# Kernel tuning notes

Hardware: AMD Instinct MI355X
Metric: run time of the kernel (lower is better)

The kernel has to match this reference:

```python
import jax, jax.numpy as jnp
import numpy as np

TEMPERATURE = 2.0


def _offdiag_idx(n):
    # flat indices of the off-diagonal entries of an [n, n] matrix, row-major,
    # reshaped to [n, n-1] (matches torch masked_select(~eye).view(n, n-1))
    idx = np.arange(n * n).reshape(n, n)
    return jnp.asarray(idx[~np.eye(n, dtype=bool)].reshape(n, n - 1))


def setup_inputs() -> dict:
    key = jax.random.key(0)
    k1, k2, k3, k4 = jax.random.split(key, 4)
    B, D = 256, 512
    return {
        "wt_emb": jax.random.normal(k1, (B, D), dtype=jnp.float32),
        "mt_emb": jax.random.normal(k2, (B, D), dtype=jnp.float32),
        "label_wt": jax.random.uniform(k3, (B,), dtype=jnp.float32),
        "label_mt": jax.random.uniform(k4, (B,), dtype=jnp.float32),
    }


def reference(wt_emb, mt_emb, label_wt, label_mt):
    t = TEMPERATURE
    features = jnp.concatenate([wt_emb, mt_emb], axis=0)            # [n, D]
    labels = jnp.concatenate([label_wt, label_mt], axis=0)[:, None]  # [n, 1]
    n = features.shape[0]

    # L1 label differences: [n, n]
    label_diffs = jnp.abs(labels[:, None, :] - labels[None, :, :]).sum(-1)

    # negative L2 feature distances (safe sqrt: diagonal is exactly 0)
    diff = features[:, None, :] - features[None, :, :]               # [n, n, D]
    sq = jnp.sum(diff * diff, axis=-1)                               # [n, n]
    dist = jnp.where(sq > 0, jnp.sqrt(jnp.where(sq > 0, sq, 1.0)), 0.0)
    logits = -dist / t
    logits = logits - jax.lax.stop_gradient(jnp.max(logits, axis=1, keepdims=True))
    exp_logits = jnp.exp(logits)

    # drop diagonal -> [n, n-1]
    off = _offdiag_idx(n)
    lo = logits.reshape(-1)[off]
    eo = exp_logits.reshape(-1)[off]
    ldo = label_diffs.reshape(-1)[off]

    # vectorized over positive index k: mask[i, k, j] = ld[i, j] >= ld[i, k]
    neg_mask = ldo[:, None, :] >= ldo[:, :, None]                    # [n, n-1, n-1]
    denom = jnp.sum(jnp.where(neg_mask, eo[:, None, :], 0.0), axis=-1)  # [n, n-1]
    pos_log_probs = lo - jnp.log(denom)                              # [n, n-1]
    return -jnp.sum(pos_log_probs) / (n * (n - 1))
```

## Files before the change

### kernel.cpp

```cpp
#include <hip/hip_runtime.h>

#define N 512
#define B 256
#define D 512
#define NT 512
#define NBLK (N / 2)

#define WS_SL    0
#define WS_NORM  512
#define WS_PART  1024
#define WS_FH    2048
#define WS_G     (2048 + (N * D) / 2)

typedef _Float16 half4_t  __attribute__((ext_vector_type(4)));
typedef _Float16 half8_t  __attribute__((ext_vector_type(8)));
typedef float    f32x4    __attribute__((ext_vector_type(4)));

__global__ __launch_bounds__(NT) void sort_rows_kernel(
    const float* __restrict__ wt, const float* __restrict__ mt,
    const float* __restrict__ lwt, const float* __restrict__ lmt,
    float* __restrict__ ws)
{
    const int t = threadIdx.x, b = blockIdx.x;
    __shared__ float slab[N];
    __shared__ int scnt[32];
    slab[t] = (t < B) ? lwt[t] : lmt[t - B];
    if (t < 32) scnt[t] = 0;
    __syncthreads();

    const int jj = t & 31, j = b * 32 + jj, c = t >> 5;
    const float lj = slab[j];
    int r = 0;
    #pragma unroll 8
    for (int x = c * 32; x < c * 32 + 32; ++x) {
        const float v = slab[x];
        r += (v < lj || (v == lj && x < j)) ? 1 : 0;
    }
    atomicAdd(&scnt[jj], r);
    __syncthreads();

    if (t < 32)
        ws[WS_SL + scnt[t]] = slab[b * 32 + t];

    const int row = b * 32 + (t >> 4), s16 = t & 15;
    const int rr = scnt[t >> 4];
    const float* F = (row < B) ? (wt + (size_t)row * D) : (mt + (size_t)(row - B) * D);
    const float4* F4 = (const float4*)F;
    half4_t* Dst = (half4_t*)((_Float16*)(ws + WS_FH) + (size_t)rr * D);
    float nacc = 0.f;
    #pragma unroll
    for (int q = 0; q < 8; ++q) {
        const int idx = s16 + 16 * q;
        const float4 v = F4[idx];
        half4_t h;
        h[0] = (_Float16)v.x; h[1] = (_Float16)v.y;
        h[2] = (_Float16)v.z; h[3] = (_Float16)v.w;
        const float f0 = (float)h[0], f1 = (float)h[1];
        const float f2 = (float)h[2], f3 = (float)h[3];
        nacc += f0 * f0 + f1 * f1 + f2 * f2 + f3 * f3;
        Dst[idx] = h;
    }
    nacc += __shfl_down(nacc, 8, 16);
    nacc += __shfl_down(nacc, 4, 16);
    nacc += __shfl_down(nacc, 2, 16);
    nacc += __shfl_down(nacc, 1, 16);
    if (s16 == 0) ws[WS_NORM + rr] = nacc;
}

__global__ __launch_bounds__(256) void gram_kernel(float* __restrict__ ws)
{
    const int lane = threadIdx.x & 63;
    const int wid  = blockIdx.x * 4 + (threadIdx.x >> 6);
    const int ti = wid >> 5, tj = wid & 31;
    const int quad = lane >> 4, m = lane & 15;

    const _Float16* Fh = (const _Float16*)(ws + WS_FH);
    const _Float16* Arow = Fh + (size_t)(ti * 16 + m) * D + quad * 8;
    const _Float16* Brow = Fh + (size_t)(tj * 16 + m) * D + quad * 8;

    f32x4 acc = {0.f, 0.f, 0.f, 0.f};
    #pragma unroll
    for (int k0 = 0; k0 < D; k0 += 32) {
        const half8_t a = *(const half8_t*)(Arow + k0);
        const half8_t b = *(const half8_t*)(Brow + k0);
        acc = __builtin_amdgcn_mfma_f32_16x16x32_f16(a, b, acc, 0, 0, 0);
    }
    float* G = ws + WS_G;
    const int col = tj * 16 + m;
    #pragma unroll
    for (int rg = 0; rg < 4; ++rg)
        G[(size_t)(ti * 16 + quad * 4 + rg) * N + col] = acc[rg];
}

__global__ __launch_bounds__(NT) void rnc_main(float* __restrict__ ws)
{
    const int b = blockIdx.x, i0 = 2 * b, i1 = 2 * b + 1;
    const int t = threadIdx.x;
    const int w = t >> 6, lane = t & 63;

    __shared__ float sl[N];
    __shared__ float snm[N];
    __shared__ __align__(16) float sp0[N];
    __shared__ __align__(16) float sf0[N];
    __shared__ __align__(16) float sp1[N];
    __shared__ __align__(16) float sf1[N];
    __shared__ float sred[NT / 64];

    sl[t]  = ws[WS_SL + t];
    snm[t] = ws[WS_NORM + t];
    __syncthreads();
    const float li0 = sl[i0], li1 = sl[i1];
    const float ni0 = snm[i0], ni1 = snm[i1];

    const float* G = ws + WS_G;
    const float g0 = G[(size_t)i0 * N + t];
    const float g1 = G[(size_t)i1 * N + t];
    const float d0 = fmaxf(ni0 + snm[t] - 2.f * g0, 0.f);
    const float d1 = fmaxf(ni1 + snm[t] - 2.f * g1, 0.f);
    const float lg0 = -0.5f * sqrtf(d0);
    const float lg1 = -0.5f * sqrtf(d1);
    float lg_acc = 0.f;
    if (t != i0) lg_acc += lg0;
    if (t != i1) lg_acc += lg1;
    const float e0 = (t == i0) ? 0.f : __expf(lg0);
    const float e1 = (t == i1) ? 0.f : __expf(lg1);
    sp0[t] = e0; sf0[t] = e0;
    sp1[t] = e1; sf1[t] = e1;
    __syncthreads();

    if (w < 4) {
        float* arr = (w == 0) ? sp0 : (w == 1) ? sf0 : (w == 2) ? sp1 : sf1;
        float4* a4 = (float4*)arr;
        float4 u0 = a4[lane * 2], u1 = a4[lane * 2 + 1];
        float v0 = u0.x, v1 = u0.y, v2 = u0.z, v3 = u0.w;
        float v4 = u1.x, v5 = u1.y, v6 = u1.z, v7 = u1.w;
        if ((w & 1) == 0) {
            v1 += v0; v2 += v1; v3 += v2; v4 += v3; v5 += v4; v6 += v5; v7 += v6;
            float x = v7;
            #pragma unroll
            for (int off = 1; off < 64; off <<= 1) {
                const float y = __shfl_up(x, off, 64);
                if (lane >= off) x += y;
            }
            float ex = __shfl_up(x, 1, 64);
            if (lane == 0) ex = 0.f;
            v0 += ex; v1 += ex; v2 += ex; v3 += ex; v4 += ex; v5 += ex; v6 += ex; v7 += ex;
        } else {
            v6 += v7; v5 += v6; v4 += v5; v3 += v4; v2 += v3; v1 += v2; v0 += v1;
            float x = v0;
            #pragma unroll
            for (int off = 1; off < 64; off <<= 1) {
                const float y = __shfl_down(x, off, 64);
                if (lane + off < 64) x += y;
            }
            float ex = __shfl_down(x, 1, 64);
            if (lane == 63) ex = 0.f;
            v0 += ex; v1 += ex; v2 += ex; v3 += ex; v4 += ex; v5 += ex; v6 += ex; v7 += ex;
        }
        a4[lane * 2]     = make_float4(v0, v1, v2, v3);
        a4[lane * 2 + 1] = make_float4(v4, v5, v6, v7);
    }
    __syncthreads();

    float local = lg_acc;
    #pragma unroll
    for (int p = 0; p < 2; ++p) {
        const int x = t;
        const int ri = p ? i1 : i0;
        const float li = p ? li1 : li0;
        const float* SP = p ? sp1 : sp0;
        const float* SF = p ? sf1 : sf0;
        if (x != ri) {
            const float th = fabsf(li - sl[x]);
            int lo = 0, hi = ri + 1;
            while (lo < hi) {
                const int mid = (lo + hi) >> 1;
                if (fabsf(li - sl[mid]) >= th) lo = mid + 1; else hi = mid;
            }
            const int a = lo;
            lo = ri + 1; hi = N;
            while (lo < hi) {
                const int mid = (lo + hi) >> 1;
                if (fabsf(li - sl[mid]) >= th) hi = mid; else lo = mid + 1;
            }
            const int bb = lo;
            const float denom = ((a > 0) ? SP[a - 1] : 0.f) + ((bb < N) ? SF[bb] : 0.f);
            local -= __logf(denom);
        }
    }

    #pragma unroll
    for (int off = 32; off > 0; off >>= 1)
        local += __shfl_down(local, off, 64);
    if (lane == 0) sred[w] = local;
    __syncthreads();
    if (t == 0) {
        float sum = 0.f;
        #pragma unroll
        for (int k = 0; k < NT / 64; ++k) sum += sred[k];
        ws[WS_PART + b] = sum;
    }
}

__global__ __launch_bounds__(NBLK) void rnc_finalize(
    const float* __restrict__ ws, float* __restrict__ out)
{
    const int t = threadIdx.x;
    __shared__ float sred[NBLK / 64];
    float v = ws[WS_PART + t];
    #pragma unroll
    for (int off = 32; off > 0; off >>= 1)
        v += __shfl_down(v, off, 64);
    if ((t & 63) == 0) sred[t >> 6] = v;
    __syncthreads();
    if (t == 0) {
        float sum = 0.f;
        #pragma unroll
        for (int k = 0; k < NBLK / 64; ++k) sum += sred[k];
        out[0] = -sum / (float)((long)N * (N - 1));
    }
}

extern "C" void kernel_launch(void* const* d_in, const int* in_sizes, int n_in,
                              void* d_out, int out_size, void* d_ws, size_t ws_size,
                              hipStream_t stream) {
    const float* wt  = (const float*)d_in[0];
    const float* mt  = (const float*)d_in[1];
    const float* lwt = (const float*)d_in[2];
    const float* lmt = (const float*)d_in[3];
    float* out = (float*)d_out;
    float* ws  = (float*)d_ws;

    sort_rows_kernel<<<16, NT, 0, stream>>>(wt, mt, lwt, lmt, ws);
    gram_kernel<<<256, 256, 0, stream>>>(ws);
    rnc_main<<<NBLK, NT, 0, stream>>>(ws);
    rnc_finalize<<<1, NBLK, 0, stream>>>(ws, out);
}
```

Measured before the change: 74.84 us.

## Fuse label sort into gram kernel and finalize via atomic last-block reduction

Merges the sort/convert kernel into the gram kernel: the gram now reads fp32 features directly, converts them to fp16 in registers, and is computed in original row order. A sorted-to-original index permutation is stored so rnc_main can gather Gram entries and take norms from the Gram diagonal. The finalize kernel is replaced by an atomic accumulate plus a last-block counter inside rnc_main, cutting four launches to two. The cost is redundant fp32 loads and conversions per tile, scattered Gram gathers, and atomics.

After: 80.30 us. 7.3% more time.

```diff
diff --git a/kernel.cpp b/kernel.cpp
--- a/kernel.cpp
+++ b/kernel.cpp
@@ -3,87 +3,80 @@
 #define N 512
 #define B 256
 #define D 512
-#define NT 512
-#define NBLK (N / 2)
-
-#define WS_SL    0
-#define WS_NORM  512
-#define WS_PART  1024
-#define WS_FH    2048
-#define WS_G     (2048 + (N * D) / 2)
-
-typedef _Float16 half4_t  __attribute__((ext_vector_type(4)));
-typedef _Float16 half8_t  __attribute__((ext_vector_type(8)));
-typedef float    f32x4    __attribute__((ext_vector_type(4)));
-
-__global__ __launch_bounds__(NT) void sort_rows_kernel(
+#define NBLK 256
+
+#define WS_SL   0
+#define WS_SO   512
+#define WS_SUM  1024
+#define WS_CNT  1025
+#define WS_G    2048
+
+typedef _Float16 half8_t __attribute__((ext_vector_type(8)));
+typedef float    f32x4  __attribute__((ext_vector_type(8 / 2)));
+
+__global__ __launch_bounds__(256) void gram_rank_kernel(
     const float* __restrict__ wt, const float* __restrict__ mt,
     const float* __restrict__ lwt, const float* __restrict__ lmt,
     float* __restrict__ ws)
 {
-    const int t = threadIdx.x, b = blockIdx.x;
-    __shared__ float slab[N];
-    __shared__ int scnt[32];
-    slab[t] = (t < B) ? lwt[t] : lmt[t - B];
-    if (t < 32) scnt[t] = 0;
-    __syncthreads();
-
-    const int jj = t & 31, j = b * 32 + jj, c = t >> 5;
-    const float lj = slab[j];
-    int r = 0;
-    #pragma unroll 8
-    for (int x = c * 32; x < c * 32 + 32; ++x) {
-        const float v = slab[x];
-        r += (v < lj || (v == lj && x < j)) ? 1 : 0;
-    }
-    atomicAdd(&scnt[jj], r);
-    __syncthreads();
-
-    if (t < 32)
-        ws[WS_SL + scnt[t]] = slab[b * 32 + t];
-
-    const int row = b * 32 + (t >> 4), s16 = t & 15;
-    const int rr = scnt[t >> 4];
-    const float* F = (row < B) ? (wt + (size_t)row * D) : (mt + (size_t)(row - B) * D);
-    const float4* F4 = (const float4*)F;
-    half4_t* Dst = (half4_t*)((_Float16*)(ws + WS_FH) + (size_t)rr * D);
-    float nacc = 0.f;
-    #pragma unroll
-    for (int q = 0; q < 8; ++q) {
-        const int idx = s16 + 16 * q;
-        const float4 v = F4[idx];
-        half4_t h;
-        h[0] = (_Float16)v.x; h[1] = (_Float16)v.y;
-        h[2] = (_Float16)v.z; h[3] = (_Float16)v.w;
-        const float f0 = (float)h[0], f1 = (float)h[1];
-        const float f2 = (float)h[2], f3 = (float)h[3];
-        nacc += f0 * f0 + f1 * f1 + f2 * f2 + f3 * f3;
-        Dst[idx] = h;
-    }
-    nacc += __shfl_down(nacc, 8, 16);
-    nacc += __shfl_down(nacc, 4, 16);
-    nacc += __shfl_down(nacc, 2, 16);
-    nacc += __shfl_down(nacc, 1, 16);
-    if (s16 == 0) ws[WS_NORM + rr] = nacc;
-}
-
-__global__ __launch_bounds__(256) void gram_kernel(float* __restrict__ ws)
-{
-    const int lane = threadIdx.x & 63;
-    const int wid  = blockIdx.x * 4 + (threadIdx.x >> 6);
+    const int t = threadIdx.x, bb = blockIdx.x;
+
+    if (bb < 16) {
+        __shared__ float slab[N];
+        __shared__ int scnt[32];
+        slab[t] = (t < B) ? lwt[t] : lmt[t - B];
+        { const int t2 = t + 256; slab[t2] = (t2 < B) ? lwt[t2] : lmt[t2 - B]; }
+        if (t < 32) scnt[t] = 0;
+        __syncthreads();
+        const int jr = t >> 3, c = t & 7;
+        const int j = bb * 32 + jr;
+        const float lj = slab[j];
+        int r = 0;
+        #pragma unroll 8
+        for (int i = 0; i < 64; ++i) {
+            const int x = c + 8 * i;
+            const float v = slab[x];
+            r += (v < lj || (v == lj && x < j)) ? 1 : 0;
+        }
+        atomicAdd(&scnt[jr], r);
+        __syncthreads();
+        if (t < 32) {
+            const int r2 = scnt[t], j2 = bb * 32 + t;
+            ws[WS_SL + r2] = slab[j2];
+            ((int*)ws)[WS_SO + r2] = j2;
+        }
+        if (bb == 0 && t == 0) {
+            ws[WS_SUM] = 0.f;
+            ((unsigned*)ws)[WS_CNT] = 0u;
+        }
+    }
+
+    const int lane = t & 63;
+    const int wid  = bb * 4 + (t >> 6);
     const int ti = wid >> 5, tj = wid & 31;
     const int quad = lane >> 4, m = lane & 15;
-
-    const _Float16* Fh = (const _Float16*)(ws + WS_FH);
-    const _Float16* Arow = Fh + (size_t)(ti * 16 + m) * D + quad * 8;
-    const _Float16* Brow = Fh + (size_t)(tj * 16 + m) * D + quad * 8;
+    const int rowA = ti * 16 + m, rowB = tj * 16 + m;
+    const float* FA = (rowA < B) ? (wt + (size_t)rowA * D) : (mt + (size_t)(rowA - B) * D);
+    const float* FB = (rowB < B) ? (wt + (size_t)rowB * D) : (mt + (size_t)(rowB - B) * D);
+    FA += quad * 8; FB += quad * 8;
 
     f32x4 acc = {0.f, 0.f, 0.f, 0.f};
     #pragma unroll
     for (int k0 = 0; k0 < D; k0 += 32) {
-        const half8_t a = *(const half8_t*)(Arow + k0);
-        const half8_t b = *(const half8_t*)(Brow + k0);
-        acc = __builtin_amdgcn_mfma_f32_16x16x32_f16(a, b, acc, 0, 0, 0);
+        const float4 fa0 = *(const float4*)(FA + k0);
+        const float4 fa1 = *(const float4*)(FA + k0 + 4);
+        const float4 fb0 = *(const float4*)(FB + k0);
+        const float4 fb1 = *(const float4*)(FB + k0 + 4);
+        half8_t a, b2;
+        a[0] = (_Float16)fa0.x; a[1] = (_Float16)fa0.y;
+        a[2] = (_Float16)fa0.z; a[3] = (_Float16)fa0.w;
+        a[4] = (_Float16)fa1.x; a[5] = (_Float16)fa1.y;
+        a[6] = (_Float16)fa1.z; a[7] = (_Float16)fa1.w;
+        b2[0] = (_Float16)fb0.x; b2[1] = (_Float16)fb0.y;
+        b2[2] = (_Float16)fb0.z; b2[3] = (_Float16)fb0.w;
+        b2[4] = (_Float16)fb1.x; b2[5] = (_Float16)fb1.y;
+        b2[6] = (_Float16)fb1.z; b2[7] = (_Float16)fb1.w;
+        acc = __builtin_amdgcn_mfma_f32_16x16x32_f16(a, b2, acc, 0, 0, 0);
     }
     float* G = ws + WS_G;
     const int col = tj * 16 + m;
@@ -92,29 +85,36 @@
         G[(size_t)(ti * 16 + quad * 4 + rg) * N + col] = acc[rg];
 }
 
-__global__ __launch_bounds__(NT) void rnc_main(float* __restrict__ ws)
+__global__ __launch_bounds__(512) void rnc_main(
+    float* __restrict__ ws, float* __restrict__ out)
 {
     const int b = blockIdx.x, i0 = 2 * b, i1 = 2 * b + 1;
     const int t = threadIdx.x;
     const int w = t >> 6, lane = t & 63;
 
     __shared__ float sl[N];
+    __shared__ int   sso[N];
     __shared__ float snm[N];
     __shared__ __align__(16) float sp0[N];
     __shared__ __align__(16) float sf0[N];
     __shared__ __align__(16) float sp1[N];
     __shared__ __align__(16) float sf1[N];
-    __shared__ float sred[NT / 64];
+    __shared__ float sred[8];
 
     sl[t]  = ws[WS_SL + t];
-    snm[t] = ws[WS_NORM + t];
-    __syncthreads();
+    sso[t] = ((const int*)ws)[WS_SO + t];
+    __syncthreads();
+
+    const float* G = ws + WS_G;
+    const int ot = sso[t];
+    snm[t] = G[(size_t)ot * N + ot];
+    const int oi0 = sso[i0], oi1 = sso[i1];
     const float li0 = sl[i0], li1 = sl[i1];
+    __syncthreads();
     const float ni0 = snm[i0], ni1 = snm[i1];
 
-    const float* G = ws + WS_G;
-    const float g0 = G[(size_t)i0 * N + t];
-    const float g1 = G[(size_t)i1 * N + t];
+    const float g0 = G[(size_t)oi0 * N + ot];
+    const float g1 = G[(size_t)oi1 * N + ot];
     const float d0 = fmaxf(ni0 + snm[t] - 2.f * g0, 0.f);
     const float d1 = fmaxf(ni1 + snm[t] - 2.f * g1, 0.f);
     const float lg0 = -0.5f * sqrtf(d0);
@@ -183,8 +183,8 @@
                 const int mid = (lo + hi) >> 1;
                 if (fabsf(li - sl[mid]) >= th) hi = mid; else lo = mid + 1;
             }
-            const int bb = lo;
-            const float denom = ((a > 0) ? SP[a - 1] : 0.f) + ((bb < N) ? SF[bb] : 0.f);
+            const int bb2 = lo;
+            const float denom = ((a > 0) ? SP[a - 1] : 0.f) + ((bb2 < N) ? SF[bb2] : 0.f);
             local -= __logf(denom);
         }
     }
@@ -197,27 +197,14 @@
     if (t == 0) {
         float sum = 0.f;
         #pragma unroll
-        for (int k = 0; k < NT / 64; ++k) sum += sred[k];
-        ws[WS_PART + b] = sum;
-    }
-}
-
-__global__ __launch_bounds__(NBLK) void rnc_finalize(
-    const float* __restrict__ ws, float* __restrict__ out)
-{
-    const int t = threadIdx.x;
-    __shared__ float sred[NBLK / 64];
-    float v = ws[WS_PART + t];
-    #pragma unroll
-    for (int off = 32; off > 0; off >>= 1)
-        v += __shfl_down(v, off, 64);
-    if ((t & 63) == 0) sred[t >> 6] = v;
-    __syncthreads();
-    if (t == 0) {
-        float sum = 0.f;
-        #pragma unroll
-        for (int k = 0; k < NBLK / 64; ++k) sum += sred[k];
-        out[0] = -sum / (float)((long)N * (N - 1));
+        for (int k = 0; k < 8; ++k) sum += sred[k];
+        atomicAdd(&ws[WS_SUM], sum);
+        __threadfence();
+        const unsigned old = atomicAdd(&((unsigned*)ws)[WS_CNT], 1u);
+        if (old == NBLK - 1) {
+            const float total = atomicAdd(&ws[WS_SUM], 0.f);
+            out[0] = -total / (float)((long)N * (N - 1));
+        }
     }
 }
 
@@ -231,8 +218,6 @@
     float* out = (float*)d_out;
     float* ws  = (float*)d_ws;
 
-    sort_rows_kernel<<<16, NT, 0, stream>>>(wt, mt, lwt, lmt, ws);
-    gram_kernel<<<256, 256, 0, stream>>>(ws);
-    rnc_main<<<NBLK, NT, 0, stream>>>(ws);
-    rnc_finalize<<<1, NBLK, 0, stream>>>(ws, out);
+    gram_rank_kernel<<<256, 256, 0, stream>>>(wt, mt, lwt, lmt, ws);
+    rnc_main<<<NBLK, 512, 0, stream>>>(ws, out);
 }
```

## Fuse all stages into one cooperative kernel with grid-wide syncs

Applied to the files above, without the earlier changes.

Merges the sort, gram, main and finalize kernels into a single cooperative launch of 256 blocks, using grid.sync() between phases instead of separate kernel launches. The rank computation is redistributed so each block ranks two labels with packed warp reductions rather than the earlier per-block atomics. The goal is to remove three launch gaps. In exchange it adds the cost of cooperative launch and grid barriers, and the gram phase uses 8 waves per block with the same MFMA tiling.

New measurement: 164.5 us. +119.8%, slower.

```diff
diff --git a/kernel.cpp b/kernel.cpp
--- a/kernel.cpp
+++ b/kernel.cpp
@@ -1,10 +1,13 @@
 #include <hip/hip_runtime.h>
+#include <hip/hip_cooperative_groups.h>
+
+namespace cg = cooperative_groups;
 
 #define N 512
 #define B 256
 #define D 512
 #define NT 512
-#define NBLK (N / 2)
+#define GRID 256
 
 #define WS_SL    0
 #define WS_NORM  512
@@ -12,212 +15,219 @@
 #define WS_FH    2048
 #define WS_G     (2048 + (N * D) / 2)
 
-typedef _Float16 half4_t  __attribute__((ext_vector_type(4)));
-typedef _Float16 half8_t  __attribute__((ext_vector_type(8)));
-typedef float    f32x4    __attribute__((ext_vector_type(4)));
-
-__global__ __launch_bounds__(NT) void sort_rows_kernel(
+typedef _Float16 half8_t __attribute__((ext_vector_type(8)));
+typedef float    f32x4   __attribute__((ext_vector_type(4)));
+
+__global__ __launch_bounds__(NT) void rnc_all(
     const float* __restrict__ wt, const float* __restrict__ mt,
     const float* __restrict__ lwt, const float* __restrict__ lmt,
-    float* __restrict__ ws)
+    float* __restrict__ ws, float* __restrict__ out)
 {
-    const int t = threadIdx.x, b = blockIdx.x;
+    cg::grid_group gridg = cg::this_grid();
+    const int b = blockIdx.x, t = threadIdx.x;
+    const int w = t >> 6, lane = t & 63;
+
     __shared__ float slab[N];
-    __shared__ int scnt[32];
-    slab[t] = (t < B) ? lwt[t] : lmt[t - B];
-    if (t < 32) scnt[t] = 0;
-    __syncthreads();
-
-    const int jj = t & 31, j = b * 32 + jj, c = t >> 5;
-    const float lj = slab[j];
-    int r = 0;
-    #pragma unroll 8
-    for (int x = c * 32; x < c * 32 + 32; ++x) {
-        const float v = slab[x];
-        r += (v < lj || (v == lj && x < j)) ? 1 : 0;
-    }
-    atomicAdd(&scnt[jj], r);
-    __syncthreads();
-
-    if (t < 32)
-        ws[WS_SL + scnt[t]] = slab[b * 32 + t];
-
-    const int row = b * 32 + (t >> 4), s16 = t & 15;
-    const int rr = scnt[t >> 4];
-    const float* F = (row < B) ? (wt + (size_t)row * D) : (mt + (size_t)(row - B) * D);
-    const float4* F4 = (const float4*)F;
-    half4_t* Dst = (half4_t*)((_Float16*)(ws + WS_FH) + (size_t)rr * D);
-    float nacc = 0.f;
-    #pragma unroll
-    for (int q = 0; q < 8; ++q) {
-        const int idx = s16 + 16 * q;
-        const float4 v = F4[idx];
-        half4_t h;
-        h[0] = (_Float16)v.x; h[1] = (_Float16)v.y;
-        h[2] = (_Float16)v.z; h[3] = (_Float16)v.w;
-        const float f0 = (float)h[0], f1 = (float)h[1];
-        const float f2 = (float)h[2], f3 = (float)h[3];
-        nacc += f0 * f0 + f1 * f1 + f2 * f2 + f3 * f3;
-        Dst[idx] = h;
-    }
-    nacc += __shfl_down(nacc, 8, 16);
-    nacc += __shfl_down(nacc, 4, 16);
-    nacc += __shfl_down(nacc, 2, 16);
-    nacc += __shfl_down(nacc, 1, 16);
-    if (s16 == 0) ws[WS_NORM + rr] = nacc;
-}
-
-__global__ __launch_bounds__(256) void gram_kernel(float* __restrict__ ws)
-{
-    const int lane = threadIdx.x & 63;
-    const int wid  = blockIdx.x * 4 + (threadIdx.x >> 6);
-    const int ti = wid >> 5, tj = wid & 31;
-    const int quad = lane >> 4, m = lane & 15;
-
-    const _Float16* Fh = (const _Float16*)(ws + WS_FH);
-    const _Float16* Arow = Fh + (size_t)(ti * 16 + m) * D + quad * 8;
-    const _Float16* Brow = Fh + (size_t)(tj * 16 + m) * D + quad * 8;
-
-    f32x4 acc = {0.f, 0.f, 0.f, 0.f};
-    #pragma unroll
-    for (int k0 = 0; k0 < D; k0 += 32) {
-        const half8_t a = *(const half8_t*)(Arow + k0);
-        const half8_t b = *(const half8_t*)(Brow + k0);
-        acc = __builtin_amdgcn_mfma_f32_16x16x32_f16(a, b, acc, 0, 0, 0);
-    }
-    float* G = ws + WS_G;
-    const int col = tj * 16 + m;
-    #pragma unroll
-    for (int rg = 0; rg < 4; ++rg)
-        G[(size_t)(ti * 16 + quad * 4 + rg) * N + col] = acc[rg];
-}
-
-__global__ __launch_bounds__(NT) void rnc_main(float* __restrict__ ws)
-{
-    const int b = blockIdx.x, i0 = 2 * b, i1 = 2 * b + 1;
-    const int t = threadIdx.x;
-    const int w = t >> 6, lane = t & 63;
-
-    __shared__ float sl[N];
     __shared__ float snm[N];
     __shared__ __align__(16) float sp0[N];
     __shared__ __align__(16) float sf0[N];
     __shared__ __align__(16) float sp1[N];
     __shared__ __align__(16) float sf1[N];
-    __shared__ float sred[NT / 64];
-
-    sl[t]  = ws[WS_SL + t];
-    snm[t] = ws[WS_NORM + t];
-    __syncthreads();
-    const float li0 = sl[i0], li1 = sl[i1];
-    const float ni0 = snm[i0], ni1 = snm[i1];
-
-    const float* G = ws + WS_G;
-    const float g0 = G[(size_t)i0 * N + t];
-    const float g1 = G[(size_t)i1 * N + t];
-    const float d0 = fmaxf(ni0 + snm[t] - 2.f * g0, 0.f);
-    const float d1 = fmaxf(ni1 + snm[t] - 2.f * g1, 0.f);
-    const float lg0 = -0.5f * sqrtf(d0);
-    const float lg1 = -0.5f * sqrtf(d1);
-    float lg_acc = 0.f;
-    if (t != i0) lg_acc += lg0;
-    if (t != i1) lg_acc += lg1;
-    const float e0 = (t == i0) ? 0.f : __expf(lg0);
-    const float e1 = (t == i1) ? 0.f : __expf(lg1);
-    sp0[t] = e0; sf0[t] = e0;
-    sp1[t] = e1; sf1[t] = e1;
-    __syncthreads();
-
-    if (w < 4) {
-        float* arr = (w == 0) ? sp0 : (w == 1) ? sf0 : (w == 2) ? sp1 : sf1;
-        float4* a4 = (float4*)arr;
-        float4 u0 = a4[lane * 2], u1 = a4[lane * 2 + 1];
-        float v0 = u0.x, v1 = u0.y, v2 = u0.z, v3 = u0.w;
-        float v4 = u1.x, v5 = u1.y, v6 = u1.z, v7 = u1.w;
-        if ((w & 1) == 0) {
-            v1 += v0; v2 += v1; v3 += v2; v4 += v3; v5 += v4; v6 += v5; v7 += v6;
-            float x = v7;
-            #pragma unroll
-            for (int off = 1; off < 64; off <<= 1) {
-                const float y = __shfl_up(x, off, 64);
-                if (lane >= off) x += y;
+    __shared__ float srA[8], srB[8];
+    __shared__ int   sri[8];
+    __shared__ int   sr01;
+
+    const int j0 = 2 * b, j1 = 2 * b + 1;
+    slab[t] = (t < B) ? lwt[t] : lmt[t - B];
+    __syncthreads();
+    const float lj0 = slab[j0], lj1 = slab[j1];
+    {
+        const float v = slab[t];
+        int c = ((v < lj0 || (v == lj0 && t < j0)) ? 1 : 0)
+              + ((v < lj1 || (v == lj1 && t < j1)) ? 0x10000 : 0);
+        #pragma unroll
+        for (int off = 32; off > 0; off >>= 1) c += __shfl_down(c, off, 64);
+        if (lane == 0) sri[w] = c;
+    }
+    __syncthreads();
+    if (t == 0) {
+        int s = 0;
+        #pragma unroll
+        for (int k = 0; k < 8; ++k) s += sri[k];
+        sr01 = s;
+    }
+    __syncthreads();
+    const int r0 = sr01 & 0xffff, r1 = sr01 >> 16;
+
+    {
+        const float* F0 = (j0 < B) ? (wt + (size_t)j0 * D) : (mt + (size_t)(j0 - B) * D);
+        const float* F1 = (j1 < B) ? (wt + (size_t)j1 * D) : (mt + (size_t)(j1 - B) * D);
+        const _Float16 h0 = (_Float16)F0[t];
+        const _Float16 h1 = (_Float16)F1[t];
+        _Float16* fh = (_Float16*)(ws + WS_FH);
+        fh[(size_t)r0 * D + t] = h0;
+        fh[(size_t)r1 * D + t] = h1;
+        float n0 = (float)h0 * (float)h0;
+        float n1 = (float)h1 * (float)h1;
+        #pragma unroll
+        for (int off = 32; off > 0; off >>= 1) {
+            n0 += __shfl_down(n0, off, 64);
+            n1 += __shfl_down(n1, off, 64);
+        }
+        if (lane == 0) { srA[w] = n0; srB[w] = n1; }
+    }
+    __syncthreads();
+    if (t == 0) {
+        float s0 = 0.f, s1 = 0.f;
+        #pragma unroll
+        for (int k = 0; k < 8; ++k) { s0 += srA[k]; s1 += srB[k]; }
+        ws[WS_NORM + r0] = s0;
+        ws[WS_NORM + r1] = s1;
+        ws[WS_SL + r0] = lj0;
+        ws[WS_SL + r1] = lj1;
+    }
+    gridg.sync();
+
+    {
+        const int wid = b * 8 + w;
+        if (wid < 1024) {
+            const int ti = wid >> 5, tj = wid & 31;
+            const int quad = lane >> 4, m = lane & 15;
+            const _Float16* fh = (const _Float16*)(ws + WS_FH);
+            const _Float16* Arow = fh + (size_t)(ti * 16 + m) * D + quad * 8;
+            const _Float16* Brow = fh + (size_t)(tj * 16 + m) * D + quad * 8;
+            f32x4 acc = {0.f, 0.f, 0.f, 0.f};
+            #pragma unroll
+            for (int k0 = 0; k0 < D; k0 += 32) {
+                const half8_t a  = *(const half8_t*)(Arow + k0);
+                const half8_t b2 = *(const half8_t*)(Brow + k0);
+                acc = __builtin_amdgcn_mfma_f32_16x16x32_f16(a, b2, acc, 0, 0, 0);
             }
-            float ex = __shfl_up(x, 1, 64);
-            if (lane == 0) ex = 0.f;
-            v0 += ex; v1 += ex; v2 += ex; v3 += ex; v4 += ex; v5 += ex; v6 += ex; v7 += ex;
-        } else {
-            v6 += v7; v5 += v6; v4 += v5; v3 += v4; v2 += v3; v1 += v2; v0 += v1;
-            float x = v0;
-            #pragma unroll
-            for (int off = 1; off < 64; off <<= 1) {
-                const float y = __shfl_down(x, off, 64);
-                if (lane + off < 64) x += y;
+            float* G = ws + WS_G;
+            const int col = tj * 16 + m;
+            #pragma unroll
+            for (int rg = 0; rg < 4; ++rg)
+                G[(size_t)(ti * 16 + quad * 4 + rg) * N + col] = acc[rg];
+        }
+    }
+    gridg.sync();
+
+    const int i0 = 2 * b, i1 = 2 * b + 1;
+    slab[t] = ws[WS_SL + t];
+    snm[t]  = ws[WS_NORM + t];
+    __syncthreads();
+    const float li0 = slab[i0], li1 = slab[i1];
+    const float ni0 = snm[i0],  ni1 = snm[i1];
+
+    {
+        const float* G = ws + WS_G;
+        const float g0 = G[(size_t)i0 * N + t];
+        const float g1 = G[(size_t)i1 * N + t];
+        const float d0 = fmaxf(ni0 + snm[t] - 2.f * g0, 0.f);
+        const float d1 = fmaxf(ni1 + snm[t] - 2.f * g1, 0.f);
+        const float lg0 = -0.5f * sqrtf(d0);
+        const float lg1 = -0.5f * sqrtf(d1);
+        float lg_acc = 0.f;
+        if (t != i0) lg_acc += lg0;
+        if (t != i1) lg_acc += lg1;
+        const float e0 = (t == i0) ? 0.f : __expf(lg0);
+        const float e1 = (t == i1) ? 0.f : __expf(lg1);
+        sp0[t] = e0; sf0[t] = e0;
+        sp1[t] = e1; sf1[t] = e1;
+        srA[0] = 0.f;
+        __syncthreads();
+
+        if (w < 4) {
+            float* arr = (w == 0) ? sp0 : (w == 1) ? sf0 : (w == 2) ? sp1 : sf1;
+            float4* a4 = (float4*)arr;
+            float4 u0 = a4[lane * 2], u1 = a4[lane * 2 + 1];
+            float v0 = u0.x, v1 = u0.y, v2 = u0.z, v3 = u0.w;
+            float v4 = u1.x, v5 = u1.y, v6 = u1.z, v7 = u1.w;
+            if ((w & 1) == 0) {
+                v1 += v0; v2 += v1; v3 += v2; v4 += v3; v5 += v4; v6 += v5; v7 += v6;
+                float x = v7;
+                #pragma unroll
+                for (int off = 1; off < 64; off <<= 1) {
+                    const float y = __shfl_up(x, off, 64);
+                    if (lane >= off) x += y;
+                }
+                float ex = __shfl_up(x, 1, 64);
+                if (lane == 0) ex = 0.f;
+                v0 += ex; v1 += ex; v2 += ex; v3 += ex;
+                v4 += ex; v5 += ex; v6 += ex; v7 += ex;
+            } else {
+                v6 += v7; v5 += v6; v4 += v5; v3 += v4; v2 += v3; v1 += v2; v0 += v1;
+                float x = v0;
+                #pragma unroll
+                for (int off = 1; off < 64; off <<= 1) {
+                    const float y = __shfl_down(x, off, 64);
+                    if (lane + off < 64) x += y;
+                }
+                float ex = __shfl_down(x, 1, 64);
+                if (lane == 63) ex = 0.f;
+                v0 += ex; v1 += ex; v2 += ex; v3 += ex;
+                v4 += ex; v5 += ex; v6 += ex; v7 += ex;
             }
-            float ex = __shfl_down(x, 1, 64);
-            if (lane == 63) ex = 0.f;
-            v0 += ex; v1 += ex; v2 += ex; v3 += ex; v4 += ex; v5 += ex; v6 += ex; v7 += ex;
-        }
-        a4[lane * 2]     = make_float4(v0, v1, v2, v3);
-        a4[lane * 2 + 1] = make_float4(v4, v5, v6, v7);
-    }
-    __syncthreads();
-
-    float local = lg_acc;
-    #pragma unroll
-    for (int p = 0; p < 2; ++p) {
-        const int x = t;
-        const int ri = p ? i1 : i0;
-        const float li = p ? li1 : li0;
-        const float* SP = p ? sp1 : sp0;
-        const float* SF = p ? sf1 : sf0;
-        if (x != ri) {
-            const float th = fabsf(li - sl[x]);
-            int lo = 0, hi = ri + 1;
-            while (lo < hi) {
-                const int mid = (lo + hi) >> 1;
-                if (fabsf(li - sl[mid]) >= th) lo = mid + 1; else hi = mid;
+            a4[lane * 2]     = make_float4(v0, v1, v2, v3);
+            a4[lane * 2 + 1] = make_float4(v4, v5, v6, v7);
+        }
+        __syncthreads();
+
+        float local = lg_acc;
+        #pragma unroll
+        for (int p = 0; p < 2; ++p) {
+            const int x = t;
+            const int ri = p ? i1 : i0;
+            const float li = p ? li1 : li0;
+            const float* SP = p ? sp1 : sp0;
+            const float* SF = p ? sf1 : sf0;
+            if (x != ri) {
+                const float th = fabsf(li - slab[x]);
+                int lo = 0, hi = ri + 1;
+                while (lo < hi) {
+                    const int mid = (lo + hi) >> 1;
+                    if (fabsf(li - slab[mid]) >= th) lo = mid + 1; else hi = mid;
+                }
+                const int a = lo;
+                lo = ri + 1; hi = N;
+                while (lo < hi) {
+                    const int mid = (lo + hi) >> 1;
+                    if (fabsf(li - slab[mid]) >= th) hi = mid; else lo = mid + 1;
+                }
+                const int bb2 = lo;
+                const float denom = ((a > 0) ? SP[a - 1] : 0.f)
+                                  + ((bb2 < N) ? SF[bb2] : 0.f);
+                local -= __logf(denom);
             }
-            const int a = lo;
-            lo = ri + 1; hi = N;
-            while (lo < hi) {
-                const int mid = (lo + hi) >> 1;
-                if (fabsf(li - sl[mid]) >= th) hi = mid; else lo = mid + 1;
-            }
-            const int bb = lo;
-            const float denom = ((a > 0) ? SP[a - 1] : 0.f) + ((bb < N) ? SF[bb] : 0.f);
-            local -= __logf(denom);
-        }
-    }
-
-    #pragma unroll
-    for (int off = 32; off > 0; off >>= 1)
-        local += __shfl_down(local, off, 64);
-    if (lane == 0) sred[w] = local;
-    __syncthreads();
-    if (t == 0) {
-        float sum = 0.f;
-        #pragma unroll
-        for (int k = 0; k < NT / 64; ++k) sum += sred[k];
-        ws[WS_PART + b] = sum;
-    }
-}
-
-__global__ __launch_bounds__(NBLK) void rnc_finalize(
-    const float* __restrict__ ws, float* __restrict__ out)
-{
-    const int t = threadIdx.x;
-    __shared__ float sred[NBLK / 64];
-    float v = ws[WS_PART + t];
-    #pragma unroll
-    for (int off = 32; off > 0; off >>= 1)
-        v += __shfl_down(v, off, 64);
-    if ((t & 63) == 0) sred[t >> 6] = v;
-    __syncthreads();
-    if (t == 0) {
-        float sum = 0.f;
-        #pragma unroll
-        for (int k = 0; k < NBLK / 64; ++k) sum += sred[k];
-        out[0] = -sum / (float)((long)N * (N - 1));
+        }
+
+        #pragma unroll
+        for (int off = 32; off > 0; off >>= 1)
+            local += __shfl_down(local, off, 64);
+        if (lane == 0) srA[w] = local;
+        __syncthreads();
+        if (t == 0) {
+            float sum = 0.f;
+            #pragma unroll
+            for (int k = 0; k < 8; ++k) sum += srA[k];
+            ws[WS_PART + b] = sum;
+        }
+    }
+    gridg.sync();
+
+    if (b == 0) {
+        float v2 = (t < GRID) ? ws[WS_PART + t] : 0.f;
+        #pragma unroll
+        for (int off = 32; off > 0; off >>= 1)
+            v2 += __shfl_down(v2, off, 64);
+        if (lane == 0) srB[w] = v2;
+        __syncthreads();
+        if (t == 0) {
+            float sum = 0.f;
+            #pragma unroll
+            for (int k = 0; k < 8; ++k) sum += srB[k];
+            out[0] = -sum / (float)((long)N * (N - 1));
+        }
     }
 }
 
@@ -231,8 +241,8 @@
     float* out = (float*)d_out;
     float* ws  = (float*)d_ws;
 
-    sort_rows_kernel<<<16, NT, 0, stream>>>(wt, mt, lwt, lmt, ws);
-    gram_kernel<<<256, 256, 0, stream>>>(ws);
-    rnc_main<<<NBLK, NT, 0, stream>>>(ws);
-    rnc_finalize<<<1, NBLK, 0, stream>>>(ws, out);
+    void* args[] = {(void*)&wt, (void*)&mt, (void*)&lwt, (void*)&lmt,
+                    (void*)&ws, (void*)&out};
+    hipLaunchCooperativeKernel((const void*)rnc_all, dim3(GRID), dim3(NT),
+                               args, 0, stream);
 }
```
